# Performance work log

Measured on AMD Instinct MI355X. Metric: run time of the kernel, lower is better.

## Reference

```python
import jax, jax.numpy as jnp
import numpy as np

CL1_K = 25
CL2_K = 25


def cheb_stack(L, x0, K):
    # x0: (V, M) -> (K, V, M) Chebyshev basis T_k(L) x0
    if K == 1:
        return x0[None]
    x1 = L @ x0
    if K == 2:
        return jnp.stack([x0, x1])

    def step(carry, _):
        xm1, xm2 = carry
        xk = 2.0 * (L @ xm1) - xm2
        return (xk, xm1), xk

    _, rest = jax.lax.scan(step, (x1, x0), None, length=K - 2)
    return jnp.concatenate([x0[None], x1[None], rest], axis=0)


def graph_conv(x, L, W, b, K):
    # x: (B, C, V) -> (B, Fout, V); matches torch Graph_Conv permute/view logic
    B, C, V = x.shape
    x0 = x.transpose(2, 1, 0).reshape(V, C * B)
    xs = cheb_stack(L, x0, K)                              # (K, V, C*B)
    xs = xs.reshape(K, V, C, B).transpose(3, 1, 2, 0)      # (B, V, C, K)
    xs = xs.reshape(B * V, C * K)
    y = xs @ W.T + b                                       # (B*V, Fout)
    return y.reshape(B, V, -1).transpose(0, 2, 1)


def maxpool4(x):
    B, C, V = x.shape
    return x.reshape(B, C, V // 4, 4).max(axis=-1)


def setup_inputs() -> dict:
    key = jax.random.key(0)
    ks = jax.random.split(key, 10)
    B, C, V, Vp = 32, 16, 4000, 4096
    CL1_F, CL2_F, FC_F = 64, 128, 10
    x = jax.random.normal(ks[0], (B, C, V), dtype=jnp.float32)
    perm = jax.random.permutation(ks[1], Vp)
    # rescaled Laplacians, scaled for stable 25-step recurrence
    L1 = jax.random.normal(ks[2], (Vp, Vp), dtype=jnp.float32) * (0.3 / np.sqrt(Vp))
    L2 = jax.random.normal(ks[3], (Vp // 4, Vp // 4), dtype=jnp.float32) * (0.3 / np.sqrt(Vp // 4))
    W1 = jax.random.normal(ks[4], (CL1_F, C * CL1_K), dtype=jnp.float32) * np.sqrt(2.0 / (C * CL1_K + CL1_F))
    b1 = jnp.zeros((CL1_F,), dtype=jnp.float32)
    W2 = jax.random.normal(ks[5], (CL2_F, CL1_F * CL2_K), dtype=jnp.float32) * np.sqrt(2.0 / (CL1_F * CL2_K + CL2_F))
    b2 = jnp.zeros((CL2_F,), dtype=jnp.float32)
    FC_IN = CL2_F * Vp // 16
    Wfc = jax.random.normal(ks[6], (FC_F, FC_IN), dtype=jnp.float32) * np.sqrt(2.0 / (FC_IN + FC_F))
    bfc = jnp.zeros((FC_F,), dtype=jnp.float32)
    return {"x": x, "perm": perm, "L1": L1, "L2": L2, "W1": W1, "b1": b1,
            "W2": W2, "b2": b2, "Wfc": Wfc, "bfc": bfc}


def reference(x, perm, L1, L2, W1, b1, W2, b2, Wfc, bfc):
    # BatchNorm1d(affine=False), training-mode batch statistics
    mu = x.mean(axis=(0, 2), keepdims=True)
    var = x.var(axis=(0, 2), keepdims=True)
    x = (x - mu) / jnp.sqrt(var + 1e-5)
    # Permute: zero-pad vertices to len(perm), then index
    B, C, V = x.shape
    Vp = perm.shape[0]
    x = jnp.pad(x, ((0, 0), (0, 0), (0, Vp - V)))[:, :, perm]
    x = jax.nn.relu(graph_conv(x, L1, W1, b1, CL1_K))
    x = maxpool4(x)
    x = jax.nn.relu(graph_conv(x, L2, W2, b2, CL2_K))
    x = maxpool4(x)
    x = x.reshape(B, -1)
    # dropout in eval mode (identity)
    return x @ Wfc.T + bfc
```

## Files before the change

kernel.cpp:

```cpp
#include <hip/hip_runtime.h>

typedef _Float16 half8 __attribute__((ext_vector_type(8)));
typedef _Float16 half4 __attribute__((ext_vector_type(4)));
typedef float f32x4 __attribute__((ext_vector_type(4)));

__device__ __forceinline__ void gload_lds16(const void* g, void* l) {
  __builtin_amdgcn_global_load_lds((const __attribute__((address_space(1))) void*)g,
                                   (__attribute__((address_space(3))) void*)l, 16, 0, 0);
}

__global__ __launch_bounds__(256) void k_bn_partial(const float* __restrict__ x,
                                                    float* __restrict__ part) {
  const int c = blockIdx.x & 15;
  const int seg = blockIdx.x >> 4;
  const int t = threadIdx.x;
  float s = 0.f, s2 = 0.f;
  for (int b = 0; b < 32; ++b) {
    const float* row = x + (size_t)(b * 16 + c) * 4000 + seg * 500;
    for (int v = t; v < 500; v += 256) {
      float val = row[v];
      s += val;
      s2 += val * val;
    }
  }
#pragma unroll
  for (int off = 32; off > 0; off >>= 1) {
    s += __shfl_down(s, off);
    s2 += __shfl_down(s2, off);
  }
  __shared__ float rs_[4], rs2_[4];
  if ((t & 63) == 0) { rs_[t >> 6] = s; rs2_[t >> 6] = s2; }
  __syncthreads();
  if (t == 0) {
    part[c * 8 + seg] = rs_[0] + rs_[1] + rs_[2] + rs_[3];
    part[128 + c * 8 + seg] = rs2_[0] + rs2_[1] + rs2_[2] + rs2_[3];
  }
}

__global__ void k_bn_final(const float* __restrict__ part, float* __restrict__ musig) {
  const int c = threadIdx.x;
  if (c < 16) {
    float S = 0.f, S2 = 0.f;
#pragma unroll
    for (int seg = 0; seg < 8; ++seg) {
      S += part[c * 8 + seg];
      S2 += part[128 + c * 8 + seg];
    }
    const float inv = 1.f / 128000.f;
    float mu = S * inv;
    float var = S2 * inv - mu * mu;
    musig[c] = mu;
    musig[16 + c] = rsqrtf(var + 1e-5f);
  }
}

__global__ __launch_bounds__(256) void k_build_x0(const float* __restrict__ x,
                                                  const int* __restrict__ perm,
                                                  const float* __restrict__ musig,
                                                  _Float16* __restrict__ X0) {
  const int idx = blockIdx.x * 256 + threadIdx.x;
  const int v = idx & 4095;
  const int m = idx >> 12;
  const int b = m & 31;
  const int c = m >> 5;
  const int pv = perm[v];
  float val = 0.f;
  if (pv < 4000)
    val = (x[((size_t)(b * 16 + c)) * 4000 + pv] - musig[c]) * musig[16 + c] * 0.0625f;
  X0[idx] = (_Float16)val;
}

__global__ __launch_bounds__(256) void k_cvt_f16(const float* __restrict__ s,
                                                 _Float16* __restrict__ d, int n) {
  const int i = (blockIdx.x * 256 + threadIdx.x) * 4;
  if (i >= n) return;
  f32x4 v = *(const f32x4*)(s + i);
  half4 h;
  h[0] = (_Float16)v[0]; h[1] = (_Float16)v[1];
  h[2] = (_Float16)v[2]; h[3] = (_Float16)v[3];
  *(half4*)(d + i) = h;
}

__global__ __launch_bounds__(256) void k_zero(_Float16* __restrict__ p, int n8) {
  const int i = blockIdx.x * 256 + threadIdx.x;
  if (i < n8) *(half8*)(p + (size_t)i * 8) = half8{};
}

__global__ __launch_bounds__(256) void k_prep_w(const float* __restrict__ W,
                                                _Float16* __restrict__ Wp,
                                                int F, int shiftC, int kround) {
  const int idx = blockIdx.x * 256 + threadIdx.x;
  const int CS = 1 << shiftC;
  const int KPtot = kround * CS;
  if (idx >= F * KPtot) return;
  const int f = idx / KPtot;
  const int rem = idx - f * KPtot;
  const int k = rem >> shiftC;
  const int c = rem & (CS - 1);
  float v = 0.f;
  if (k < 25) v = W[(size_t)f * (CS * 25) + c * 25 + k];
  Wp[idx] = (_Float16)v;
}

__global__ __launch_bounds__(256, 2) void k_cheb1b(const _Float16* __restrict__ Xprev,
                                                   const _Float16* __restrict__ Lm,
                                                   _Float16* __restrict__ P) {
  __shared__ _Float16 lds[4][8192];
  const int t = threadIdx.x;
  const int lane = t & 63;
  const int ln = lane & 15;
  const int g = lane >> 4;
  const int w = t >> 6;
  const int wm = w >> 1, wn = w & 1;
  const int bid = blockIdx.x;
  const int kq = bid & 3;
  const int bx = (bid >> 2) & 31;
  const int by = bid >> 7;
  const int v0 = bx * 128, m0 = by * 128;
  const size_t rs = 8192;

  const char* Ag = (const char*)Xprev + (size_t)m0 * rs + kq * 2048;
  const char* Bg = (const char*)Lm + (size_t)v0 * rs + kq * 2048;

  f32x4 acc[4][4] = {};

  auto stage = [&](int buf, int tt) {
    char* A = (char*)&lds[buf][0];
    char* B = (char*)&lds[buf][4096];
#pragma unroll
    for (int j = 0; j < 2; ++j) {
      const int ch = j * 256 + t;
      const int row = ch >> 2, c8 = ch & 3;
      const size_t so = (size_t)row * rs + tt * 64 + ((c8 ^ ((row >> 1) & 3)) << 4);
      gload_lds16(Ag + so, A + ch * 16);
      gload_lds16(Bg + so, B + ch * 16);
    }
  };

  stage(0, 0);
  stage(1, 1);
  stage(2, 2);
  asm volatile("s_waitcnt vmcnt(8)" ::: "memory");
  asm volatile("s_barrier" ::: "memory");

  for (int tt = 0; tt < 32; ++tt) {
    const int cur = tt & 3;
    const char* A = (const char*)&lds[cur][0];
    const char* B = A + 8192;
    half8 a[4], b[4];
#pragma unroll
    for (int mi = 0; mi < 4; ++mi) {
      const int ar = wm * 64 + mi * 16 + ln;
      a[mi] = *(const half8*)(A + ar * 64 + ((g ^ ((ar >> 1) & 3)) << 4));
    }
#pragma unroll
    for (int ni = 0; ni < 4; ++ni) {
      const int br = wn * 64 + ni * 16 + ln;
      b[ni] = *(const half8*)(B + br * 64 + ((g ^ ((br >> 1) & 3)) << 4));
    }
    if (tt + 3 < 32) {
      stage((tt + 3) & 3, tt + 3);
      asm volatile("s_waitcnt vmcnt(8)" ::: "memory");
    } else if (tt + 2 < 32) {
      asm volatile("s_waitcnt vmcnt(4)" ::: "memory");
    } else {
      asm volatile("s_waitcnt vmcnt(0)" ::: "memory");
    }
    asm volatile("s_barrier" ::: "memory");
    asm volatile("s_waitcnt lgkmcnt(0)" ::: "memory");
    __builtin_amdgcn_sched_barrier(0);
    __builtin_amdgcn_s_setprio(1);
#pragma unroll
    for (int mi = 0; mi < 4; ++mi)
#pragma unroll
      for (int ni = 0; ni < 4; ++ni)
        acc[mi][ni] = __builtin_amdgcn_mfma_f32_16x16x32_f16(a[mi], b[ni], acc[mi][ni], 0, 0, 0);
    __builtin_amdgcn_s_setprio(0);
    asm volatile("s_barrier" ::: "memory");
  }

  _Float16* Pq = P + (size_t)kq * 2097152;
#pragma unroll
  for (int mi = 0; mi < 4; ++mi) {
#pragma unroll
    for (int ni = 0; ni < 4; ++ni) {
      const int vv = v0 + wn * 64 + ni * 16 + ln;
      const int mmb = m0 + wm * 64 + mi * 16 + g * 4;
#pragma unroll
      for (int r = 0; r < 4; ++r)
        Pq[(size_t)(mmb + r) * 4096 + vv] = (_Float16)acc[mi][ni][r];
    }
  }
}

__global__ __launch_bounds__(256) void k_cheb_red4(const _Float16* __restrict__ P,
                                                   const _Float16* __restrict__ Xm2,
                                                   _Float16* __restrict__ Xout,
                                                   float alpha, float beta) {
  const size_t i = ((size_t)blockIdx.x * 256 + threadIdx.x) * 8;
  float s[8] = {};
#pragma unroll
  for (int p = 0; p < 4; ++p) {
    half8 v = *(const half8*)(P + (size_t)p * 2097152 + i);
#pragma unroll
    for (int j = 0; j < 8; ++j) s[j] += (float)v[j];
  }
  half8 xm2 = {};
  if (beta != 0.f) xm2 = *(const half8*)(Xm2 + i);
  half8 o;
#pragma unroll
  for (int j = 0; j < 8; ++j) o[j] = (_Float16)(alpha * s[j] - beta * (float)xm2[j]);
  *(half8*)(Xout + i) = o;
}

__global__ __launch_bounds__(256, 2) void k_cheb2(const _Float16* __restrict__ Xprev,
                                                  const _Float16* __restrict__ Lm,
                                                  const _Float16* __restrict__ Xm2,
                                                  _Float16* __restrict__ Xout,
                                                  float alpha, float beta) {
  __shared__ _Float16 lds[3][8192];
  const int t = threadIdx.x;
  const int lane = t & 63;
  const int ln = lane & 15;
  const int g = lane >> 4;
  const int g16 = g << 4;
  const int w = t >> 6;
  const int wm = w >> 1, wn = w & 1;
  const int bx = blockIdx.x & 15;
  const int by = blockIdx.x >> 4;
  const int v0 = bx * 64, m0 = by * 64;
  const size_t rs = 2048;

  const char* Ag = (const char*)Xprev + (size_t)m0 * rs;
  const char* Bg = (const char*)Lm + (size_t)v0 * rs;

  f32x4 acc[2][2] = {};

  auto stageHalf = [&](int buf, int tt, int half) {
    const char* src = (half == 0) ? Ag : Bg;
    char* dst0 = (char*)&lds[buf][0] + half * 8192;
#pragma unroll
    for (int j = 0; j < 2; ++j) {
      const int idx = j * 256 + t;
      const int row = idx >> 3, c8 = idx & 7;
      gload_lds16(src + (size_t)row * rs + tt * 128 + ((c8 ^ (row & 7)) << 4),
                  dst0 + idx * 16);
    }
  };

  stageHalf(0, 0, 0); stageHalf(0, 0, 1);
  stageHalf(1, 1, 0); stageHalf(1, 1, 1);
  asm volatile("s_waitcnt vmcnt(4)" ::: "memory");
  asm volatile("s_barrier" ::: "memory");

  for (int tt = 0; tt < 16; ++tt) {
    const int cur = tt % 3;
    const int nxt = (tt + 2) % 3;
    const char* A = (const char*)&lds[cur][0];
    const char* B = A + 8192;
    half8 a[2][2], b[2][2];
#pragma unroll
    for (int kk = 0; kk < 2; ++kk) {
#pragma unroll
      for (int mi = 0; mi < 2; ++mi) {
        const int ar = wm * 32 + mi * 16 + ln;
        a[kk][mi] = *(const half8*)(A + ar * 128 + ((kk * 64 + g16) ^ ((ar & 7) << 4)));
      }
#pragma unroll
      for (int ni = 0; ni < 2; ++ni) {
        const int br = wn * 32 + ni * 16 + ln;
        b[kk][ni] = *(const half8*)(B + br * 128 + ((kk * 64 + g16) ^ ((br & 7) << 4)));
      }
    }
    if (tt + 2 < 16) {
      stageHalf(nxt, tt + 2, 0);
      stageHalf(nxt, tt + 2, 1);
      asm volatile("s_waitcnt vmcnt(4)" ::: "memory");
    } else {
      asm volatile("s_waitcnt vmcnt(0)" ::: "memory");
    }
    asm volatile("s_barrier" ::: "memory");
    asm volatile("s_waitcnt lgkmcnt(0)" ::: "memory");
    __builtin_amdgcn_sched_barrier(0);
    __builtin_amdgcn_s_setprio(1);
#pragma unroll
    for (int kk = 0; kk < 2; ++kk)
#pragma unroll
      for (int mi = 0; mi < 2; ++mi)
#pragma unroll
        for (int ni = 0; ni < 2; ++ni)
          acc[mi][ni] = __builtin_amdgcn_mfma_f32_16x16x32_f16(a[kk][mi], b[kk][ni],
                                                               acc[mi][ni], 0, 0, 0);
    __builtin_amdgcn_s_setprio(0);
    asm volatile("s_barrier" ::: "memory");
  }

#pragma unroll
  for (int mi = 0; mi < 2; ++mi) {
#pragma unroll
    for (int ni = 0; ni < 2; ++ni) {
      const int vv = v0 + wn * 32 + ni * 16 + ln;
      const int mmb = m0 + wm * 32 + mi * 16 + g * 4;
#pragma unroll
      for (int r = 0; r < 4; ++r) {
        const size_t idx = (size_t)(mmb + r) * 1024 + vv;
        float val = alpha * acc[mi][ni][r];
        if (beta != 0.f) val -= (float)Xm2[idx];
        Xout[idx] = (_Float16)val;
      }
    }
  }
}

template <int FT, int MODE>
__global__ __launch_bounds__(256, 2) void k_dense(const _Float16* __restrict__ Wp,
                                                  const _Float16* __restrict__ XS,
                                                  const float* __restrict__ bias,
                                                  void* __restrict__ outp,
                                                  int Vv, int shiftC, int nsteps,
                                                  int k0plane, float ascale, float bscale) {
  __shared__ _Float16 Alds[2][FT * 64];
  __shared__ _Float16 Blds[2][64 * 64];
  const int t = threadIdx.x;
  const int lane = t & 63;
  const int ln = lane & 15;
  const int g = lane >> 4;
  const int w = t >> 6;
  const int wf = w >> 1, wn = w & 1;
  const int f0w = wf * (FT / 2);
  const int n0w = wn * 32;
  const int n0 = blockIdx.x * 64;
  const int b = n0 / Vv;
  const int vb = n0 % Vv;
  const int Kp = nsteps * 64;
  const int cmask = (1 << shiftC) - 1;
  const size_t plane = 2097152;
  constexpr int NM = FT / 32;

  f32x4 acc[NM][2] = {};

  auto stageA = [&](int buf, int s) {
    const int q0 = s * 64;
    char* A = (char*)&Alds[buf][0];
#pragma unroll
    for (int j = 0; j < FT / 32; ++j) {
      const int ch = j * 256 + t;
      const int f = ch >> 3, c8 = ch & 7;
      gload_lds16((const char*)Wp + ((size_t)f * Kp + q0) * 2 + ((c8 ^ (f & 7)) << 4),
                  A + ch * 16);
    }
  };
  auto loadB = [&](int s, half8* r) {
    const int q0 = s * 64;
#pragma unroll
    for (int j = 0; j < 2; ++j) {
      const int idx = j * 256 + t;
      const int q = idx >> 3, n8 = idx & 7;
      const int qq = q0 + q;
      int k = qq >> shiftC;
      const int c = qq & cmask;
      if (k == 0) k = k0plane;
      r[j] = *(const half8*)(XS + (size_t)k * plane + (size_t)(c * 32 + b) * Vv + vb + n8 * 8);
    }
  };
  auto writeB = [&](int buf, const half8* r) {
#pragma unroll
    for (int j = 0; j < 2; ++j) {
      const int idx = j * 256 + t;
      const int q = idx >> 3, n8 = idx & 7;
#pragma unroll
      for (int e = 0; e < 8; ++e) {
        const int n = n8 * 8 + e;
        Blds[buf][n * 64 + ((((q >> 3) ^ (n >> 3) ^ (n & 7))) << 3) + (q & 7)] = r[j][e];
      }
    }
  };

  half8 rb[2];
  stageA(0, 0);
  loadB(0, rb);
  writeB(0, rb);
  asm volatile("s_waitcnt vmcnt(0)" ::: "memory");
  __syncthreads();

  for (int s = 0; s < nsteps; ++s) {
    const int cur = s & 1;
    const bool more = (s + 1 < nsteps);
    if (more) {
      stageA(cur ^ 1, s + 1);
      loadB(s + 1, rb);
    }
    const _Float16* A = &Alds[cur][0];
    const _Float16* B = &Blds[cur][0];
#pragma unroll
    for (int kk = 0; kk < 2; ++kk) {
      half8 af[NM], bf[2];
#pragma unroll
      for (int mi = 0; mi < NM; ++mi) {
        const int fr = f0w + mi * 16 + ln;
        af[mi] = *(const half8*)((const char*)A + fr * 128 +
                                 ((kk * 64 + g * 16) ^ ((fr & 7) << 4)));
      }
#pragma unroll
      for (int ni = 0; ni < 2; ++ni) {
        const int n = n0w + ni * 16 + ln;
        bf[ni] = *(const half8*)((const char*)B + n * 128 +
                                 ((((kk * 4 + g) ^ (n >> 3) ^ (n & 7))) << 4));
      }
#pragma unroll
      for (int mi = 0; mi < NM; ++mi)
#pragma unroll
        for (int ni = 0; ni < 2; ++ni)
          acc[mi][ni] = __builtin_amdgcn_mfma_f32_16x16x32_f16(af[mi], bf[ni], acc[mi][ni], 0, 0, 0);
    }
    if (more) {
      writeB(cur ^ 1, rb);
      asm volatile("s_waitcnt vmcnt(0)" ::: "memory");
      __syncthreads();
    }
  }

  const bool writer = (lane & 3) == 0;
#pragma unroll
  for (int mi = 0; mi < NM; ++mi) {
#pragma unroll
    for (int ni = 0; ni < 2; ++ni) {
#pragma unroll
      for (int r = 0; r < 4; ++r) {
        const int f = f0w + mi * 16 + g * 4 + r;
        const int v = vb + n0w + ni * 16 + ln;
        float val = fmaxf(ascale * acc[mi][ni][r] + bscale * bias[f], 0.f);
        val = fmaxf(val, __shfl_xor(val, 1));
        val = fmaxf(val, __shfl_xor(val, 2));
        if (writer) {
          if constexpr (MODE == 1) {
            _Float16* Xp = (_Float16*)outp;
            Xp[(size_t)(f * 32 + b) * 1024 + (v >> 2)] = (_Float16)(val * 0.015625f);
          } else {
            float* p2o = (float*)outp;
            p2o[(size_t)b * 32768 + f * 256 + (v >> 2)] = val;
          }
        }
      }
    }
  }
}

__global__ __launch_bounds__(256) void k_fc_part(const float* __restrict__ p2,
                                                 const float* __restrict__ Wfc,
                                                 float* __restrict__ partF) {
  const int b = blockIdx.x >> 3;
  const int seg = blockIdx.x & 7;
  const int t = threadIdx.x;
  const int lane = t & 63;
  const int w = t >> 6;
  const int base = seg * 4096;
  float acc[10];
#pragma unroll
  for (int o = 0; o < 10; ++o) acc[o] = 0.f;
  const float* pb = p2 + (size_t)b * 32768 + base;
  for (int i = t; i < 4096; i += 256) {
    float p = pb[i];
#pragma unroll
    for (int o = 0; o < 10; ++o) acc[o] += p * Wfc[(size_t)o * 32768 + base + i];
  }
#pragma unroll
  for (int off = 32; off > 0; off >>= 1)
#pragma unroll
    for (int o = 0; o < 10; ++o) acc[o] += __shfl_down(acc[o], off);
  __shared__ float rws[10][4];
  if (lane == 0) {
#pragma unroll
    for (int o = 0; o < 10; ++o) rws[o][w] = acc[o];
  }
  __syncthreads();
  if (t < 10) partF[blockIdx.x * 10 + t] =
      rws[t][0] + rws[t][1] + rws[t][2] + rws[t][3];
}

__global__ void k_fc_final(const float* __restrict__ partF,
                           const float* __restrict__ bfc,
                           float* __restrict__ out) {
  const int t = threadIdx.x;
  if (t < 320) {
    const int b = t / 10, o = t - b * 10;
    float s = 0.f;
#pragma unroll
    for (int seg = 0; seg < 8; ++seg) s += partF[(b * 8 + seg) * 10 + o];
    out[b * 10 + o] = 64.f * s + bfc[o];
  }
}

extern "C" void kernel_launch(void* const* d_in, const int* in_sizes, int n_in,
                              void* d_out, int out_size, void* d_ws, size_t ws_size,
                              hipStream_t stream) {
  (void)in_sizes; (void)n_in; (void)out_size; (void)ws_size;
  const float* x = (const float*)d_in[0];
  const int* perm = (const int*)d_in[1];
  const float* L1 = (const float*)d_in[2];
  const float* L2 = (const float*)d_in[3];
  const float* W1 = (const float*)d_in[4];
  const float* b1 = (const float*)d_in[5];
  const float* W2 = (const float*)d_in[6];
  const float* b2 = (const float*)d_in[7];
  const float* Wfc = (const float*)d_in[8];
  const float* bfc = (const float*)d_in[9];
  float* out = (float*)d_out;

  char* ws = (char*)d_ws;
  size_t off = 0;
  auto alloc = [&](size_t bytes) {
    char* p = ws + off;
    off += (bytes + 255) & ~(size_t)255;
    return p;
  };
  _Float16* L1h = (_Float16*)alloc(16777216ull * 2);
  _Float16* L2h = (_Float16*)alloc(1048576ull * 2);
  _Float16* W1p = (_Float16*)alloc(64ull * 448 * 2);
  _Float16* W2p = (_Float16*)alloc(128ull * 1664 * 2);
  float* part = (float*)alloc(256 * 4);
  float* musig = (float*)alloc(32 * 4);
  float* partF = (float*)alloc(2560 * 4);
  _Float16* XS = (_Float16*)alloc(29ull * 2097152 * 2);
  float* Yt = (float*)alloc(64ull * 131072 * 4);
  float* p2 = (float*)alloc(32ull * 128 * 256 * 4);
  _Float16* Pq = (_Float16*)Yt;

  const size_t plane = 2097152;

  k_cvt_f16<<<16384, 256, 0, stream>>>(L1, L1h, 16777216);
  k_cvt_f16<<<1024, 256, 0, stream>>>(L2, L2h, 1048576);
  k_prep_w<<<112, 256, 0, stream>>>(W1, W1p, 64, 4, 28);
  k_prep_w<<<832, 256, 0, stream>>>(W2, W2p, 128, 6, 26);
  k_zero<<<3072, 256, 0, stream>>>(XS + 25 * plane, 786432);
  k_bn_partial<<<128, 256, 0, stream>>>(x, part);
  k_bn_final<<<1, 64, 0, stream>>>(part, musig);
  k_build_x0<<<8192, 256, 0, stream>>>(x, perm, musig, XS);

  for (int k = 1; k < 25; ++k) {
    k_cheb1b<<<512, 256, 0, stream>>>(XS + (size_t)(k - 1) * plane, L1h, Pq);
    k_cheb_red4<<<1024, 256, 0, stream>>>(
        Pq, XS + (size_t)(k >= 2 ? k - 2 : 0) * plane, XS + (size_t)k * plane,
        (k == 1) ? 1.f : 2.f, (k == 1) ? 0.f : 1.f);
  }
  k_dense<64, 1><<<dim3(2048, 1), 256, 0, stream>>>(W1p, XS, b1, XS + 28 * plane,
                                                    4096, 4, 7, 0, 16.f, 1.f);
  auto Xp = [&](int k) { return XS + (size_t)((k == 0) ? 28 : k) * plane; };
  for (int k = 1; k < 25; ++k) {
    k_cheb2<<<512, 256, 0, stream>>>(
        Xp(k - 1), L2h, Xp(k >= 2 ? k - 2 : 0), Xp(k),
        (k == 1) ? 1.f : 2.f, (k == 1) ? 0.f : 1.f);
  }
  k_dense<128, 2><<<dim3(512, 1), 256, 0, stream>>>(W2p, XS, b2, p2,
                                                    1024, 6, 26, 28, 1.f, 0.015625f);
  k_fc_part<<<256, 256, 0, stream>>>(p2, Wfc, partF);
  k_fc_final<<<1, 320, 0, stream>>>(partF, bfc, out);
}
```

Before: 1.172 ms.

## Replace split-K layer-1 Chebyshev GEMM and reduction with generalized fused-epilogue kernel

Removes the layer-1 path that split K four ways into 128x128 tiles, wrote fp16 partial sums and reduced them in a separate kernel. Both layers now use one 64x64-tile kernel parameterized by V and K-loop length, with the 2*L*x - x_prev recurrence fused into the epilogue. This drops the partial-sum round trip, one launch per step and the extra workspace buffer. In exchange, layer 1 uses smaller tiles over the full 4096-long K loop, which lowers data reuse per block and lengthens each block's serial work.

```diff
diff --git a/kernel.cpp b/kernel.cpp
--- a/kernel.cpp
+++ b/kernel.cpp
@@ -102,122 +102,11 @@
   Wp[idx] = (_Float16)v;
 }
 
-__global__ __launch_bounds__(256, 2) void k_cheb1b(const _Float16* __restrict__ Xprev,
-                                                   const _Float16* __restrict__ Lm,
-                                                   _Float16* __restrict__ P) {
-  __shared__ _Float16 lds[4][8192];
-  const int t = threadIdx.x;
-  const int lane = t & 63;
-  const int ln = lane & 15;
-  const int g = lane >> 4;
-  const int w = t >> 6;
-  const int wm = w >> 1, wn = w & 1;
-  const int bid = blockIdx.x;
-  const int kq = bid & 3;
-  const int bx = (bid >> 2) & 31;
-  const int by = bid >> 7;
-  const int v0 = bx * 128, m0 = by * 128;
-  const size_t rs = 8192;
-
-  const char* Ag = (const char*)Xprev + (size_t)m0 * rs + kq * 2048;
-  const char* Bg = (const char*)Lm + (size_t)v0 * rs + kq * 2048;
-
-  f32x4 acc[4][4] = {};
-
-  auto stage = [&](int buf, int tt) {
-    char* A = (char*)&lds[buf][0];
-    char* B = (char*)&lds[buf][4096];
-#pragma unroll
-    for (int j = 0; j < 2; ++j) {
-      const int ch = j * 256 + t;
-      const int row = ch >> 2, c8 = ch & 3;
-      const size_t so = (size_t)row * rs + tt * 64 + ((c8 ^ ((row >> 1) & 3)) << 4);
-      gload_lds16(Ag + so, A + ch * 16);
-      gload_lds16(Bg + so, B + ch * 16);
-    }
-  };
-
-  stage(0, 0);
-  stage(1, 1);
-  stage(2, 2);
-  asm volatile("s_waitcnt vmcnt(8)" ::: "memory");
-  asm volatile("s_barrier" ::: "memory");
-
-  for (int tt = 0; tt < 32; ++tt) {
-    const int cur = tt & 3;
-    const char* A = (const char*)&lds[cur][0];
-    const char* B = A + 8192;
-    half8 a[4], b[4];
-#pragma unroll
-    for (int mi = 0; mi < 4; ++mi) {
-      const int ar = wm * 64 + mi * 16 + ln;
-      a[mi] = *(const half8*)(A + ar * 64 + ((g ^ ((ar >> 1) & 3)) << 4));
-    }
-#pragma unroll
-    for (int ni = 0; ni < 4; ++ni) {
-      const int br = wn * 64 + ni * 16 + ln;
-      b[ni] = *(const half8*)(B + br * 64 + ((g ^ ((br >> 1) & 3)) << 4));
-    }
-    if (tt + 3 < 32) {
-      stage((tt + 3) & 3, tt + 3);
-      asm volatile("s_waitcnt vmcnt(8)" ::: "memory");
-    } else if (tt + 2 < 32) {
-      asm volatile("s_waitcnt vmcnt(4)" ::: "memory");
-    } else {
-      asm volatile("s_waitcnt vmcnt(0)" ::: "memory");
-    }
-    asm volatile("s_barrier" ::: "memory");
-    asm volatile("s_waitcnt lgkmcnt(0)" ::: "memory");
-    __builtin_amdgcn_sched_barrier(0);
-    __builtin_amdgcn_s_setprio(1);
-#pragma unroll
-    for (int mi = 0; mi < 4; ++mi)
-#pragma unroll
-      for (int ni = 0; ni < 4; ++ni)
-        acc[mi][ni] = __builtin_amdgcn_mfma_f32_16x16x32_f16(a[mi], b[ni], acc[mi][ni], 0, 0, 0);
-    __builtin_amdgcn_s_setprio(0);
-    asm volatile("s_barrier" ::: "memory");
-  }
-
-  _Float16* Pq = P + (size_t)kq * 2097152;
-#pragma unroll
-  for (int mi = 0; mi < 4; ++mi) {
-#pragma unroll
-    for (int ni = 0; ni < 4; ++ni) {
-      const int vv = v0 + wn * 64 + ni * 16 + ln;
-      const int mmb = m0 + wm * 64 + mi * 16 + g * 4;
-#pragma unroll
-      for (int r = 0; r < 4; ++r)
-        Pq[(size_t)(mmb + r) * 4096 + vv] = (_Float16)acc[mi][ni][r];
-    }
-  }
-}
-
-__global__ __launch_bounds__(256) void k_cheb_red4(const _Float16* __restrict__ P,
-                                                   const _Float16* __restrict__ Xm2,
-                                                   _Float16* __restrict__ Xout,
-                                                   float alpha, float beta) {
-  const size_t i = ((size_t)blockIdx.x * 256 + threadIdx.x) * 8;
-  float s[8] = {};
-#pragma unroll
-  for (int p = 0; p < 4; ++p) {
-    half8 v = *(const half8*)(P + (size_t)p * 2097152 + i);
-#pragma unroll
-    for (int j = 0; j < 8; ++j) s[j] += (float)v[j];
-  }
-  half8 xm2 = {};
-  if (beta != 0.f) xm2 = *(const half8*)(Xm2 + i);
-  half8 o;
-#pragma unroll
-  for (int j = 0; j < 8; ++j) o[j] = (_Float16)(alpha * s[j] - beta * (float)xm2[j]);
-  *(half8*)(Xout + i) = o;
-}
-
-__global__ __launch_bounds__(256, 2) void k_cheb2(const _Float16* __restrict__ Xprev,
+__global__ __launch_bounds__(256, 2) void k_chebf(const _Float16* __restrict__ Xprev,
                                                   const _Float16* __restrict__ Lm,
                                                   const _Float16* __restrict__ Xm2,
                                                   _Float16* __restrict__ Xout,
-                                                  float alpha, float beta) {
+                                                  int V, int NT, float alpha, float beta) {
   __shared__ _Float16 lds[3][8192];
   const int t = threadIdx.x;
   const int lane = t & 63;
@@ -226,10 +115,9 @@
   const int g16 = g << 4;
   const int w = t >> 6;
   const int wm = w >> 1, wn = w & 1;
-  const int bx = blockIdx.x & 15;
-  const int by = blockIdx.x >> 4;
-  const int v0 = bx * 64, m0 = by * 64;
-  const size_t rs = 2048;
+  const int v0 = blockIdx.x * 64;
+  const int m0 = blockIdx.y * 64;
+  const size_t rs = (size_t)V * 2;
 
   const char* Ag = (const char*)Xprev + (size_t)m0 * rs;
   const char* Bg = (const char*)Lm + (size_t)v0 * rs;
@@ -253,7 +141,7 @@
   asm volatile("s_waitcnt vmcnt(4)" ::: "memory");
   asm volatile("s_barrier" ::: "memory");
 
-  for (int tt = 0; tt < 16; ++tt) {
+  for (int tt = 0; tt < NT; ++tt) {
     const int cur = tt % 3;
     const int nxt = (tt + 2) % 3;
     const char* A = (const char*)&lds[cur][0];
@@ -272,7 +160,7 @@
         b[kk][ni] = *(const half8*)(B + br * 128 + ((kk * 64 + g16) ^ ((br & 7) << 4)));
       }
     }
-    if (tt + 2 < 16) {
+    if (tt + 2 < NT) {
       stageHalf(nxt, tt + 2, 0);
       stageHalf(nxt, tt + 2, 1);
       asm volatile("s_waitcnt vmcnt(4)" ::: "memory");
@@ -303,7 +191,7 @@
       const int mmb = m0 + wm * 32 + mi * 16 + g * 4;
 #pragma unroll
       for (int r = 0; r < 4; ++r) {
-        const size_t idx = (size_t)(mmb + r) * 1024 + vv;
+        const size_t idx = (size_t)(mmb + r) * V + vv;
         float val = alpha * acc[mi][ni][r];
         if (beta != 0.f) val -= (float)Xm2[idx];
         Xout[idx] = (_Float16)val;
@@ -522,9 +410,7 @@
   float* musig = (float*)alloc(32 * 4);
   float* partF = (float*)alloc(2560 * 4);
   _Float16* XS = (_Float16*)alloc(29ull * 2097152 * 2);
-  float* Yt = (float*)alloc(64ull * 131072 * 4);
   float* p2 = (float*)alloc(32ull * 128 * 256 * 4);
-  _Float16* Pq = (_Float16*)Yt;
 
   const size_t plane = 2097152;
 
@@ -538,18 +424,18 @@
   k_build_x0<<<8192, 256, 0, stream>>>(x, perm, musig, XS);
 
   for (int k = 1; k < 25; ++k) {
-    k_cheb1b<<<512, 256, 0, stream>>>(XS + (size_t)(k - 1) * plane, L1h, Pq);
-    k_cheb_red4<<<1024, 256, 0, stream>>>(
-        Pq, XS + (size_t)(k >= 2 ? k - 2 : 0) * plane, XS + (size_t)k * plane,
-        (k == 1) ? 1.f : 2.f, (k == 1) ? 0.f : 1.f);
+    k_chebf<<<dim3(64, 8), 256, 0, stream>>>(
+        XS + (size_t)(k - 1) * plane, L1h,
+        XS + (size_t)(k >= 2 ? k - 2 : 0) * plane, XS + (size_t)k * plane,
+        4096, 64, (k == 1) ? 1.f : 2.f, (k == 1) ? 0.f : 1.f);
   }
   k_dense<64, 1><<<dim3(2048, 1), 256, 0, stream>>>(W1p, XS, b1, XS + 28 * plane,
                                                     4096, 4, 7, 0, 16.f, 1.f);
   auto Xp = [&](int k) { return XS + (size_t)((k == 0) ? 28 : k) * plane; };
   for (int k = 1; k < 25; ++k) {
-    k_cheb2<<<512, 256, 0, stream>>>(
+    k_chebf<<<dim3(16, 32), 256, 0, stream>>>(
         Xp(k - 1), L2h, Xp(k >= 2 ? k - 2 : 0), Xp(k),
-        (k == 1) ? 1.f : 2.f, (k == 1) ? 0.f : 1.f);
+        1024, 16, (k == 1) ? 1.f : 2.f, (k == 1) ? 0.f : 1.f);
   }
   k_dense<128, 2><<<dim3(512, 1), 256, 0, stream>>>(W2p, XS, b2, p2,
                                                     1024, 6, 26, 28, 1.f, 0.015625f);
```

Result: slower. 1.200 ms (+2.4%).

## Retile layer-1 Chebyshev GEMM to 128x256 tiles with 512 threads and triple buffering

Applied to the files above, without the earlier changes.

Replaces the 128x128, 256-thread split-K kernel with a 128x256-tile, 512-thread (8-wave) kernel. It uses 128-byte K-slices, a 3-stage LDS ring, and staging issued in halves interleaved with the MFMA sub-steps. The larger tile raises arithmetic intensity and halves the block count to 256 while keeping a 4-way K split. The cost is more LDS per block, occupancy limited to one block per CU, and a more complex wait/barrier schedule.

```diff
diff --git a/kernel.cpp b/kernel.cpp
--- a/kernel.cpp
+++ b/kernel.cpp
@@ -102,81 +102,92 @@
   Wp[idx] = (_Float16)v;
 }
 
-__global__ __launch_bounds__(256, 2) void k_cheb1b(const _Float16* __restrict__ Xprev,
-                                                   const _Float16* __restrict__ Lm,
-                                                   _Float16* __restrict__ P) {
-  __shared__ _Float16 lds[4][8192];
+__global__ __launch_bounds__(512, 1) void k_cheb8(const _Float16* __restrict__ Xprev,
+                                                  const _Float16* __restrict__ Lm,
+                                                  _Float16* __restrict__ P,
+                                                  int V, int NT, int bxbits, int bybits) {
+  __shared__ _Float16 lds[3][24576];
   const int t = threadIdx.x;
   const int lane = t & 63;
   const int ln = lane & 15;
   const int g = lane >> 4;
+  const int g16 = g << 4;
   const int w = t >> 6;
-  const int wm = w >> 1, wn = w & 1;
+  const int wm = w >> 2, wn = w & 3;
   const int bid = blockIdx.x;
-  const int kq = bid & 3;
-  const int bx = (bid >> 2) & 31;
-  const int by = bid >> 7;
-  const int v0 = bx * 128, m0 = by * 128;
-  const size_t rs = 8192;
-
-  const char* Ag = (const char*)Xprev + (size_t)m0 * rs + kq * 2048;
-  const char* Bg = (const char*)Lm + (size_t)v0 * rs + kq * 2048;
+  const int bx = bid & ((1 << bxbits) - 1);
+  const int by = (bid >> bxbits) & ((1 << bybits) - 1);
+  const int kq = bid >> (bxbits + bybits);
+  const int v0 = bx * 256, m0 = by * 128;
+  const size_t rs = (size_t)V * 2;
+  const int koffB = kq * NT * 128;
+
+  const char* Ag = (const char*)Xprev + (size_t)m0 * rs + koffB;
+  const char* Bg = (const char*)Lm + (size_t)v0 * rs + koffB;
 
   f32x4 acc[4][4] = {};
 
-  auto stage = [&](int buf, int tt) {
-    char* A = (char*)&lds[buf][0];
-    char* B = (char*)&lds[buf][4096];
-#pragma unroll
-    for (int j = 0; j < 2; ++j) {
-      const int ch = j * 256 + t;
-      const int row = ch >> 2, c8 = ch & 3;
-      const size_t so = (size_t)row * rs + tt * 64 + ((c8 ^ ((row >> 1) & 3)) << 4);
-      gload_lds16(Ag + so, A + ch * 16);
-      gload_lds16(Bg + so, B + ch * 16);
+  auto stageHalf = [&](int buf, int tt, int half) {
+    char* Lb = (char*)&lds[buf][0];
+#pragma unroll
+    for (int j = 0; j < 3; ++j) {
+      const int idx = half * 1536 + j * 512 + t;
+      if (idx < 1024) {
+        const int row = idx >> 3, c8 = idx & 7;
+        gload_lds16(Ag + (size_t)row * rs + tt * 128 + ((c8 ^ (row & 7)) << 4),
+                    Lb + idx * 16);
+      } else {
+        const int bi = idx - 1024;
+        const int row = bi >> 3, c8 = bi & 7;
+        gload_lds16(Bg + (size_t)row * rs + tt * 128 + ((c8 ^ (row & 7)) << 4),
+                    Lb + 16384 + bi * 16);
+      }
     }
   };
 
-  stage(0, 0);
-  stage(1, 1);
-  stage(2, 2);
-  asm volatile("s_waitcnt vmcnt(8)" ::: "memory");
+  stageHalf(0, 0, 0); stageHalf(0, 0, 1);
+  stageHalf(1, 1, 0); stageHalf(1, 1, 1);
+  asm volatile("s_waitcnt vmcnt(6)" ::: "memory");
   asm volatile("s_barrier" ::: "memory");
 
-  for (int tt = 0; tt < 32; ++tt) {
-    const int cur = tt & 3;
+  for (int tt = 0; tt < NT; ++tt) {
+    const int cur = tt % 3;
+    const int nxt = (tt + 2) % 3;
     const char* A = (const char*)&lds[cur][0];
-    const char* B = A + 8192;
-    half8 a[4], b[4];
-#pragma unroll
-    for (int mi = 0; mi < 4; ++mi) {
-      const int ar = wm * 64 + mi * 16 + ln;
-      a[mi] = *(const half8*)(A + ar * 64 + ((g ^ ((ar >> 1) & 3)) << 4));
-    }
-#pragma unroll
-    for (int ni = 0; ni < 4; ++ni) {
-      const int br = wn * 64 + ni * 16 + ln;
-      b[ni] = *(const half8*)(B + br * 64 + ((g ^ ((br >> 1) & 3)) << 4));
-    }
-    if (tt + 3 < 32) {
-      stage((tt + 3) & 3, tt + 3);
-      asm volatile("s_waitcnt vmcnt(8)" ::: "memory");
-    } else if (tt + 2 < 32) {
-      asm volatile("s_waitcnt vmcnt(4)" ::: "memory");
-    } else {
-      asm volatile("s_waitcnt vmcnt(0)" ::: "memory");
-    }
-    asm volatile("s_barrier" ::: "memory");
-    asm volatile("s_waitcnt lgkmcnt(0)" ::: "memory");
-    __builtin_amdgcn_sched_barrier(0);
-    __builtin_amdgcn_s_setprio(1);
-#pragma unroll
-    for (int mi = 0; mi < 4; ++mi)
-#pragma unroll
-      for (int ni = 0; ni < 4; ++ni)
-        acc[mi][ni] = __builtin_amdgcn_mfma_f32_16x16x32_f16(a[mi], b[ni], acc[mi][ni], 0, 0, 0);
-    __builtin_amdgcn_s_setprio(0);
-    asm volatile("s_barrier" ::: "memory");
+    const char* B = A + 16384;
+#pragma unroll
+    for (int kk = 0; kk < 2; ++kk) {
+      half8 a[4], b[4];
+#pragma unroll
+      for (int mi = 0; mi < 4; ++mi) {
+        const int ar = wm * 64 + mi * 16 + ln;
+        a[mi] = *(const half8*)(A + ar * 128 + ((kk * 64 + g16) ^ ((ar & 7) << 4)));
+      }
+#pragma unroll
+      for (int ni = 0; ni < 4; ++ni) {
+        const int br = wn * 64 + ni * 16 + ln;
+        b[ni] = *(const half8*)(B + br * 128 + ((kk * 64 + g16) ^ ((br & 7) << 4)));
+      }
+      if (tt + 2 < NT) stageHalf(nxt, tt + 2, kk);
+      if (kk == 1) {
+        if (tt + 2 < NT) {
+          asm volatile("s_waitcnt vmcnt(6)" ::: "memory");
+        } else {
+          asm volatile("s_waitcnt vmcnt(0)" ::: "memory");
+        }
+      }
+      asm volatile("s_barrier" ::: "memory");
+      asm volatile("s_waitcnt lgkmcnt(0)" ::: "memory");
+      __builtin_amdgcn_sched_barrier(0);
+      __builtin_amdgcn_s_setprio(1);
+#pragma unroll
+      for (int mi = 0; mi < 4; ++mi)
+#pragma unroll
+        for (int ni = 0; ni < 4; ++ni)
+          acc[mi][ni] = __builtin_amdgcn_mfma_f32_16x16x32_f16(a[mi], b[ni], acc[mi][ni], 0, 0, 0);
+      __builtin_amdgcn_s_setprio(0);
+      asm volatile("s_barrier" ::: "memory");
+    }
   }
 
   _Float16* Pq = P + (size_t)kq * 2097152;
@@ -188,7 +199,7 @@
       const int mmb = m0 + wm * 64 + mi * 16 + g * 4;
 #pragma unroll
       for (int r = 0; r < 4; ++r)
-        Pq[(size_t)(mmb + r) * 4096 + vv] = (_Float16)acc[mi][ni][r];
+        Pq[(size_t)(mmb + r) * V + vv] = (_Float16)acc[mi][ni][r];
     }
   }
 }
@@ -522,9 +533,8 @@
   float* musig = (float*)alloc(32 * 4);
   float* partF = (float*)alloc(2560 * 4);
   _Float16* XS = (_Float16*)alloc(29ull * 2097152 * 2);
-  float* Yt = (float*)alloc(64ull * 131072 * 4);
+  _Float16* Pq = (_Float16*)alloc(4ull * 2097152 * 2);
   float* p2 = (float*)alloc(32ull * 128 * 256 * 4);
-  _Float16* Pq = (_Float16*)Yt;
 
   const size_t plane = 2097152;
 
@@ -538,7 +548,7 @@
   k_build_x0<<<8192, 256, 0, stream>>>(x, perm, musig, XS);
 
   for (int k = 1; k < 25; ++k) {
-    k_cheb1b<<<512, 256, 0, stream>>>(XS + (size_t)(k - 1) * plane, L1h, Pq);
+    k_cheb8<<<256, 512, 0, stream>>>(XS + (size_t)(k - 1) * plane, L1h, Pq, 4096, 16, 4, 2);
     k_cheb_red4<<<1024, 256, 0, stream>>>(
         Pq, XS + (size_t)(k >= 2 ? k - 2 : 0) * plane, XS + (size_t)k * plane,
         (k == 1) ? 1.f : 2.f, (k == 1) ? 0.f : 1.f);
```

New measurement: 1.127 ms. 3.8% less time.
